# Optimization experiments

Measured on AMD Instinct MI355X. Metric: run time of the kernel, lower is better.

The kernel has to match this reference:

```python
import jax, jax.numpy as jnp
import numpy as np

B, N, T, D = 4, 256, 64, 128
DR, DH = 32, 128  # d_relation, d_hidden


def setup_inputs() -> dict:
    key = jax.random.key(0)
    ks = jax.random.split(key, 12)
    s = 0.05
    return {
        "H": jax.random.normal(ks[0], (B, N, T, D), jnp.float32),
        "R": jax.random.normal(ks[1], (B, N, N, DR), jnp.float32),
        "delta_H": jax.random.normal(ks[2], (B, N, T, D), jnp.float32),
        # params (torch Linear convention: W @ x + b with W shape (out, in))
        "Wq": jax.random.normal(ks[3], (DH, D), jnp.float32) * s,
        "bq": jnp.zeros((DH,), jnp.float32),
        "Wk": jax.random.normal(ks[4], (DH, D), jnp.float32) * s,
        "bk": jnp.zeros((DH,), jnp.float32),
        "Wr": jax.random.normal(ks[5], (DH, DR), jnp.float32) * s,
        "br": jnp.zeros((DH,), jnp.float32),
        "Wf": jax.random.normal(ks[6], (D, 3 * D + DR), jnp.float32) * s,
        "bf": jnp.zeros((D,), jnp.float32),
        "gamma": jnp.ones((D,), jnp.float32),
        "beta": jnp.zeros((D,), jnp.float32),
    }


def reference(H, R, delta_H, Wq, bq, Wk, bk, Wr, br, Wf, bf, gamma, beta):
    Bm, Nn, Tt, Dd = H.shape
    dr = R.shape[-1]

    # projections (eval mode: dropout is identity)
    q = jnp.einsum('bitd,hd->bith', H, Wq) + bq           # (B,N,T,DH)
    k = jnp.einsum('bjtd,hd->bjth', H, Wk) + bk           # (B,N,T,DH)
    rproj = jnp.einsum('bijr,hr->bijh', R, Wr) + br       # (B,N,N,DH)

    # attn_score[b,i,j,t] = <q_i[t], k_j[t] + Wr(r_ij)> / sqrt(d_model)
    scores = (jnp.einsum('bith,bjth->bijt', q, k)
              + jnp.einsum('bith,bijh->bijt', q, rproj)) / jnp.sqrt(jnp.asarray(Dd, H.dtype))
    w = jax.nn.softmax(scores, axis=-1)                   # softmax over time t
    # exclude the j == i pair (original loop skips it)
    w = w * (1.0 - jnp.eye(Nn, dtype=w.dtype))[None, :, :, None]

    # fuse Linear decomposed over the concat [h_i, h_j, r_ij, sum_t delta_h_j]
    W1 = Wf[:, :Dd]                 # acts on h_i
    W2 = Wf[:, Dd:2 * Dd]           # acts on h_j
    W3 = Wf[:, 2 * Dd:2 * Dd + dr]  # acts on r_ij
    W4 = Wf[:, 2 * Dd + dr:]        # acts on delta sum

    A = jnp.einsum('bitd,ed->bite', H, W1)                       # (B,N,T,D)
    Bj = jnp.einsum('bjtd,ed->bjte', H, W2)                      # (B,N,T,D)
    Cij = jnp.einsum('bijr,er->bije', R, W3)                     # (B,N,N,D)
    Ej = jnp.einsum('bjd,ed->bje', delta_H.sum(axis=2), W4)      # (B,N,D)

    wsum = w.sum(axis=2)                                         # (B,N,T)
    z = ((A + bf) * wsum[..., None]
         + jnp.einsum('bijt,bjte->bite', w, Bj)
         + jnp.einsum('bijt,bije->bite', w, Cij)
         + jnp.einsum('bijt,bje->bite', w, Ej))

    # residual + LayerNorm over last dim
    x = H + z
    mu = x.mean(axis=-1, keepdims=True)
    var = x.var(axis=-1, keepdims=True)
    return (x - mu) / jnp.sqrt(var + 1e-5) * gamma + beta
```

## Files before the change

kernel.cpp:

```cpp
#include <hip/hip_runtime.h>

typedef __attribute__((ext_vector_type(4))) float f32x4;
typedef __attribute__((ext_vector_type(8))) short short8;

constexpr int NB = 4, NS = 256, NT = 64, ND = 128, NR = 32;
constexpr int WFR = 3 * ND + NR;
constexpr float SCALE = 0.08838834764831845f;

__device__ __forceinline__ unsigned short f2bf(float f) {
  unsigned x = __float_as_uint(f);
  return (unsigned short)((x + 0x7FFFu + ((x >> 16) & 1u)) >> 16);
}
__device__ __forceinline__ float bf2f(unsigned short u) {
  return __uint_as_float((unsigned)u << 16);
}

__global__ __launch_bounds__(256) void kPrep(
    const float* __restrict__ Wq, const float* __restrict__ Wk,
    const float* __restrict__ Wr, const float* __restrict__ br,
    const float* __restrict__ bq, const float* __restrict__ Wf,
    const float* __restrict__ dH, const float* __restrict__ R,
    unsigned short* __restrict__ Wqb, unsigned short* __restrict__ Wkb,
    unsigned short* __restrict__ W1b, unsigned short* __restrict__ W2b,
    unsigned short* __restrict__ W3b, unsigned short* __restrict__ Wqrt,
    float* __restrict__ Gbias, float* __restrict__ Ej,
    unsigned short* __restrict__ Rb, unsigned short* __restrict__ Rtb) {
  __shared__ __align__(16) char smem[17408];
  const int blk = blockIdx.x, tid = threadIdx.x;
  if (blk < 116) {
    if (blk < 64) {
      const int which = blk >> 4;
      const int idx = ((blk & 15) * 256 + tid) * 4;
      const int e = idx >> 7, d = idx & 127;
      float4 v;
      unsigned short* dst;
      if (which == 0)      { v = *(const float4*)&Wq[idx];            dst = Wqb; }
      else if (which == 1) { v = *(const float4*)&Wk[idx];            dst = Wkb; }
      else if (which == 2) { v = *(const float4*)&Wf[e * WFR + d];        dst = W1b; }
      else                 { v = *(const float4*)&Wf[e * WFR + ND + d];   dst = W2b; }
      dst[idx + 0] = f2bf(v.x); dst[idx + 1] = f2bf(v.y);
      dst[idx + 2] = f2bf(v.z); dst[idx + 3] = f2bf(v.w);
    } else if (blk < 68) {
      const int idx = ((blk - 64) * 256 + tid) * 4;
      const int e = idx >> 5, r = idx & 31;
      float4 v = *(const float4*)&Wf[e * WFR + 2 * ND + r];
      W3b[idx + 0] = f2bf(v.x); W3b[idx + 1] = f2bf(v.y);
      W3b[idx + 2] = f2bf(v.z); W3b[idx + 3] = f2bf(v.w);
    } else {
      const int rr = blk - 68;
      float* Vl = (float*)smem;
      float* gbl = Vl + 128;
      if (tid < 128) {
        float v = 0.f;
        if (rr < 32) v = Wr[tid * 32 + rr];
        else if (rr == 32) v = br[tid];
        Vl[tid] = v;
        gbl[tid] = bq[tid] * v;
      }
      __syncthreads();
      if (tid < 128) {
        float acc = 0.f;
        #pragma unroll 8
        for (int h = 0; h < 128; ++h) acc += Wq[h * 128 + tid] * Vl[h];
        Wqrt[rr * 128 + tid] = f2bf(acc * SCALE);
      }
      if (tid == 0) {
        float g = 0.f;
        for (int h = 0; h < 128; ++h) g += gbl[h];
        Gbias[rr] = g * SCALE;
      }
    }
  } else if (blk < 628) {
    float* ds = (float*)smem;
    const int half = tid >> 7, d = tid & 127;
    const int bj = (blk - 116) * 2 + half;
    const float* p = dH + (size_t)bj * NT * ND + d;
    float s = 0.f;
    #pragma unroll 8
    for (int t = 0; t < NT; ++t) s += p[t * ND];
    ds[half * 128 + d] = s;
    __syncthreads();
    const float* w4 = Wf + (size_t)d * WFR + 2 * ND + NR;
    float acc = 0.f;
    #pragma unroll 8
    for (int dd = 0; dd < ND; ++dd) acc += ds[half * 128 + dd] * w4[dd];
    Ej[(size_t)bj * ND + d] = acc;
  } else {
    unsigned short* rt = (unsigned short*)smem;
    const int bi = blk - 628;
    const float* src = R + (size_t)bi * 8192;
    #pragma unroll
    for (int it = 0; it < 8; ++it) {
      const int idx = (tid + it * 256) * 4;
      const float4 v = *(const float4*)&src[idx];
      const unsigned short s0 = f2bf(v.x), s1 = f2bf(v.y);
      const unsigned short s2 = f2bf(v.z), s3 = f2bf(v.w);
      unsigned long long p = (unsigned long long)s0 | ((unsigned long long)s1 << 16)
                           | ((unsigned long long)s2 << 32) | ((unsigned long long)s3 << 48);
      *(unsigned long long*)&Rb[(size_t)bi * 8192 + idx] = p;
      const int j = idx >> 5, r = idx & 31;
      *(unsigned*)&rt[j * 34 + r]     = (unsigned)s0 | ((unsigned)s1 << 16);
      *(unsigned*)&rt[j * 34 + r + 2] = (unsigned)s2 | ((unsigned)s3 << 16);
    }
    __syncthreads();
    #pragma unroll
    for (int it = 0; it < 4; ++it) {
      const int flat = (tid + it * 256) * 8;
      const int r = flat >> 8, j0 = flat & 255;
      short8 o;
      #pragma unroll
      for (int u = 0; u < 8; ++u) o[u] = (short)rt[(j0 + u) * 34 + r];
      *(short8*)&Rtb[(size_t)bi * 8192 + flat] = o;
    }
  }
}

__device__ __forceinline__ void gemm_tile(const short8 (&afr)[4][4],
    const unsigned short* __restrict__ Wp, int nt, int l15, int l4,
    f32x4 (&acc)[4]) {
  #pragma unroll
  for (int mt = 0; mt < 4; ++mt) acc[mt] = (f32x4){0.f, 0.f, 0.f, 0.f};
  #pragma unroll
  for (int kt = 0; kt < 4; ++kt) {
    short8 bfr = *(const short8*)(Wp + (16 * nt + l15) * 128 + 32 * kt + 8 * l4);
    #pragma unroll
    for (int mt = 0; mt < 4; ++mt)
      acc[mt] = __builtin_amdgcn_mfma_f32_16x16x32_bf16(afr[mt][kt], bfr, acc[mt], 0, 0, 0);
  }
}

__device__ __forceinline__ void gemm_tile2(const short8 (&afr)[2][4],
    const unsigned short* __restrict__ Wp, int nt, int l15, int l4,
    f32x4 (&acc)[2]) {
  #pragma unroll
  for (int mt = 0; mt < 2; ++mt) acc[mt] = (f32x4){0.f, 0.f, 0.f, 0.f};
  #pragma unroll
  for (int kt = 0; kt < 4; ++kt) {
    short8 bfr = *(const short8*)(Wp + (16 * nt + l15) * 128 + 32 * kt + 8 * l4);
    #pragma unroll
    for (int mt = 0; mt < 2; ++mt)
      acc[mt] = __builtin_amdgcn_mfma_f32_16x16x32_bf16(afr[mt][kt], bfr, acc[mt], 0, 0, 0);
  }
}

__global__ __launch_bounds__(256) void kB(const float* __restrict__ H,
    const unsigned short* __restrict__ W1b, const unsigned short* __restrict__ W2b,
    const unsigned short* __restrict__ Wqrt, const float* __restrict__ Gbias,
    const float* __restrict__ bf, const float* __restrict__ Ej,
    unsigned short* __restrict__ Apbb, unsigned short* __restrict__ BEb,
    unsigned short* __restrict__ Gb, unsigned short* __restrict__ Ht) {
  __shared__ unsigned short st[2][64 * 136];
  const int bn = blockIdx.x, tid = threadIdx.x;
  const int b = bn >> 8, n = bn & 255;
  const int lane = tid & 63, wv = tid >> 6;
  const int l15 = lane & 15, l4 = lane >> 4;
  short8 afr[4][4];
  const float* hb = H + (size_t)bn * (NT * ND);
  #pragma unroll
  for (int mt = 0; mt < 4; ++mt)
    #pragma unroll
    for (int kt = 0; kt < 4; ++kt) {
      const float* p = hb + (16 * mt + l15) * ND + 32 * kt + 8 * l4;
      float4 u0 = *(const float4*)p;
      float4 u1 = *(const float4*)(p + 4);
      short8 f;
      f[0] = (short)f2bf(u0.x); f[1] = (short)f2bf(u0.y);
      f[2] = (short)f2bf(u0.z); f[3] = (short)f2bf(u0.w);
      f[4] = (short)f2bf(u1.x); f[5] = (short)f2bf(u1.y);
      f[6] = (short)f2bf(u1.z); f[7] = (short)f2bf(u1.w);
      afr[mt][kt] = f;
    }
  f32x4 acc[4];
  #pragma unroll 1
  for (int pass = 0; pass < 2; ++pass) {
    const unsigned short* W = (pass == 0) ? W1b : W2b;
    unsigned short* buf = st[pass];
    #pragma unroll
    for (int n2 = 0; n2 < 2; ++n2) {
      const int nt = 2 * wv + n2, c = 16 * nt + l15;
      gemm_tile(afr, W, nt, l15, l4, acc);
      const float bias = (pass == 0) ? bf[c] : Ej[(size_t)bn * 128 + c];
      #pragma unroll
      for (int mt = 0; mt < 4; ++mt)
        #pragma unroll
        for (int jr = 0; jr < 4; ++jr)
          buf[(16 * mt + 4 * l4 + jr) * 136 + c] = f2bf(acc[mt][jr] + bias);
    }
  }
  if (wv < 3) {
    const int nt = wv, c = 16 * nt + l15;
    gemm_tile(afr, Wqrt, nt, l15, l4, acc);
    const float bias = Gbias[c];
    #pragma unroll
    for (int mt = 0; mt < 4; ++mt)
      #pragma unroll
      for (int jr = 0; jr < 4; ++jr) {
        const int tr = 16 * mt + 4 * l4 + jr;
        Gb[(size_t)bn * 3072 + tr * 48 + c] = f2bf(acc[mt][jr] + bias);
      }
  }
  __syncthreads();
  #pragma unroll
  for (int it = 0; it < 4; ++it) {
    const int flat = tid * 8 + it * 2048;
    const int row = flat >> 7, col = flat & 127;
    *(short8*)&Apbb[(size_t)bn * 8192 + flat] = *(const short8*)&st[0][row * 136 + col];
    *(short8*)&BEb[((size_t)(b * 64 + row) * 256 + n) * 128 + col] =
        *(const short8*)&st[1][row * 136 + col];
  }
  __syncthreads();
  if (wv == 0) {
    #pragma unroll
    for (int mt = 0; mt < 4; ++mt)
      #pragma unroll
      for (int kt = 0; kt < 4; ++kt)
        *(short8*)&st[0][(16 * mt + l15) * 136 + 32 * kt + 8 * l4] = afr[mt][kt];
  }
  __syncthreads();
  #pragma unroll
  for (int it = 0; it < 4; ++it) {
    const int flat = tid * 8 + it * 2048;
    const int row = flat >> 7, col = flat & 127;
    *(short8*)&Ht[((size_t)(b * 64 + row) * 256 + n) * 128 + col] =
        *(const short8*)&st[0][row * 136 + col];
  }
}

__global__ __launch_bounds__(512) void kQK(const unsigned short* __restrict__ Ht,
    const unsigned short* __restrict__ Wqb, const unsigned short* __restrict__ Wkb,
    const float* __restrict__ bq, const float* __restrict__ bk,
    unsigned short* __restrict__ Sb) {
  __shared__ unsigned short qs[256 * 136];
  __shared__ unsigned short ks[256 * 136];
  const int bt = blockIdx.x;
  const int tid = threadIdx.x, lane = tid & 63, wv = tid >> 6;
  const int l15 = lane & 15, l4 = lane >> 4;
  const unsigned short* hsrc = Ht + (size_t)bt * (256 * 128);
  short8 afr[2][4];
  #pragma unroll
  for (int mt = 0; mt < 2; ++mt)
    #pragma unroll
    for (int kt = 0; kt < 4; ++kt) {
      const int n = 32 * wv + 16 * mt + l15;
      afr[mt][kt] = *(const short8*)(hsrc + n * 128 + 32 * kt + 8 * l4);
    }
  f32x4 acc[2];
  #pragma unroll 1
  for (int pass = 0; pass < 2; ++pass) {
    const unsigned short* W = (pass == 0) ? Wqb : Wkb;
    const float* bp = (pass == 0) ? bq : bk;
    unsigned short* dst = (pass == 0) ? qs : ks;
    #pragma unroll
    for (int nt = 0; nt < 8; ++nt) {
      gemm_tile2(afr, W, nt, l15, l4, acc);
      const int c = 16 * nt + l15;
      const float bias = bp[c];
      #pragma unroll
      for (int mt = 0; mt < 2; ++mt)
        #pragma unroll
        for (int jr = 0; jr < 4; ++jr)
          dst[(32 * wv + 16 * mt + 4 * l4 + jr) * 136 + c] = f2bf(acc[mt][jr] + bias);
    }
  }
  __syncthreads();
  short8 qa[2][4];
  #pragma unroll
  for (int mt = 0; mt < 2; ++mt)
    #pragma unroll
    for (int kt = 0; kt < 4; ++kt)
      qa[mt][kt] = *(const short8*)&qs[(32 * wv + 16 * mt + l15) * 136 + 32 * kt + 8 * l4];
  unsigned short* buf = qs + wv * (32 * 136);
  #pragma unroll 1
  for (int jh = 0; jh < 2; ++jh) {
    f32x4 sacc[2][8];
    #pragma unroll
    for (int mi = 0; mi < 2; ++mi)
      #pragma unroll
      for (int ntj = 0; ntj < 8; ++ntj) sacc[mi][ntj] = (f32x4){0.f, 0.f, 0.f, 0.f};
    #pragma unroll
    for (int kt = 0; kt < 4; ++kt) {
      short8 bb[8];
      #pragma unroll
      for (int ntj = 0; ntj < 8; ++ntj)
        bb[ntj] = *(const short8*)&ks[(16 * (8 * jh + ntj) + l15) * 136 + 32 * kt + 8 * l4];
      #pragma unroll
      for (int mi = 0; mi < 2; ++mi)
        #pragma unroll
        for (int ntj = 0; ntj < 8; ++ntj)
          sacc[mi][ntj] = __builtin_amdgcn_mfma_f32_16x16x32_bf16(qa[mi][kt], bb[ntj], sacc[mi][ntj], 0, 0, 0);
    }
    #pragma unroll
    for (int mi = 0; mi < 2; ++mi)
      #pragma unroll
      for (int ntj = 0; ntj < 8; ++ntj)
        #pragma unroll
        for (int jr = 0; jr < 4; ++jr)
          buf[(16 * mi + 4 * l4 + jr) * 136 + 16 * ntj + l15] =
              f2bf(sacc[mi][ntj][jr] * SCALE);
    #pragma unroll
    for (int it = 0; it < 8; ++it) {
      const int flat = lane * 8 + it * 512;
      const int row = flat >> 7, col = flat & 127;
      *(short8*)&Sb[((size_t)bt * 256 + 32 * wv + row) * 256 + 128 * jh + col] =
          *(const short8*)&buf[row * 136 + col];
    }
  }
}

__global__ __launch_bounds__(256) void kSM(
    const unsigned short* __restrict__ Gb, const unsigned short* __restrict__ Rb,
    const unsigned short* __restrict__ Rtb, const unsigned short* __restrict__ Sb,
    const unsigned short* __restrict__ W3b, const unsigned short* __restrict__ Apbb,
    unsigned short* __restrict__ Zt, unsigned short* __restrict__ Wbw) {
  __shared__ unsigned short wl[64 * 264];
  __shared__ unsigned short Ml[4][16 * 40];
  __shared__ float wred[4][64];
  __shared__ float wsl[64];
  const int bi = blockIdx.x, b = bi >> 8, i = bi & 255;
  const int tid = threadIdx.x, lane = tid & 63, wv = tid >> 6;
  const int l15 = lane & 15, l4 = lane >> 4;
  const f32x4 zz = (f32x4){0.f, 0.f, 0.f, 0.f};

  #pragma unroll
  for (int it = 0; it < 8; ++it) {
    const int flat = tid * 8 + it * 2048;
    const int t = flat >> 8, col = flat & 255;
    *(short8*)&wl[t * 264 + col] =
        *(const short8*)&Sb[(((size_t)b * 64 + t) * 256 + i) * 256 + col];
  }

  short8 ga[4];
  #pragma unroll
  for (int mt = 0; mt < 4; ++mt)
    ga[mt] = *(const short8*)(Gb + ((size_t)bi * 64 + 16 * mt + l15) * 48 + 8 * l4);
  f32x4 acc[4][4];
  #pragma unroll
  for (int nt = 0; nt < 4; ++nt) {
    const int j = 64 * wv + 16 * nt + l15;
    short8 rb = *(const short8*)(Rb + ((size_t)bi * 256 + j) * 32 + 8 * l4);
    #pragma unroll
    for (int mt = 0; mt < 4; ++mt)
      acc[mt][nt] = __builtin_amdgcn_mfma_f32_16x16x32_bf16(ga[mt], rb, zz, 0, 0, 0);
  }
  float qbr[4][4];
  #pragma unroll
  for (int mt = 0; mt < 4; ++mt)
    #pragma unroll
    for (int jr = 0; jr < 4; ++jr)
      qbr[mt][jr] = bf2f(Gb[((size_t)bi * 64 + 16 * mt + 4 * l4 + jr) * 48 + 32]);

  __syncthreads();

  #pragma unroll
  for (int mt = 0; mt < 4; ++mt)
    #pragma unroll
    for (int nt = 0; nt < 4; ++nt)
      #pragma unroll
      for (int jr = 0; jr < 4; ++jr)
        acc[mt][nt][jr] += bf2f(wl[(16 * mt + 4 * l4 + jr) * 264 + 64 * wv + 16 * nt + l15])
                         + qbr[mt][jr];

  #pragma unroll
  for (int nt = 0; nt < 4; ++nt) {
    float mx = -1e30f;
    #pragma unroll
    for (int mt = 0; mt < 4; ++mt)
      #pragma unroll
      for (int jr = 0; jr < 4; ++jr) mx = fmaxf(mx, acc[mt][nt][jr]);
    mx = fmaxf(mx, __shfl_xor(mx, 16));
    mx = fmaxf(mx, __shfl_xor(mx, 32));
    float sm = 0.f;
    #pragma unroll
    for (int mt = 0; mt < 4; ++mt)
      #pragma unroll
      for (int jr = 0; jr < 4; ++jr) {
        const float e = __expf(acc[mt][nt][jr] - mx);
        acc[mt][nt][jr] = e;
        sm += e;
      }
    sm += __shfl_xor(sm, 16);
    sm += __shfl_xor(sm, 32);
    const int j = 64 * wv + 16 * nt + l15;
    const float inv = (j == i) ? 0.f : 1.f / sm;
    #pragma unroll
    for (int mt = 0; mt < 4; ++mt)
      #pragma unroll
      for (int jr = 0; jr < 4; ++jr) acc[mt][nt][jr] *= inv;
  }

  float part[4][4];
  #pragma unroll
  for (int mt = 0; mt < 4; ++mt)
    #pragma unroll
    for (int jr = 0; jr < 4; ++jr) {
      float s = 0.f;
      #pragma unroll
      for (int nt = 0; nt < 4; ++nt) s += acc[mt][nt][jr];
      part[mt][jr] = s;
    }
  #pragma unroll
  for (int m = 1; m < 16; m <<= 1)
    #pragma unroll
    for (int mt = 0; mt < 4; ++mt)
      #pragma unroll
      for (int jr = 0; jr < 4; ++jr) part[mt][jr] += __shfl_xor(part[mt][jr], m);
  if (l15 == 0) {
    #pragma unroll
    for (int mt = 0; mt < 4; ++mt)
      #pragma unroll
      for (int jr = 0; jr < 4; ++jr) wred[wv][16 * mt + 4 * l4 + jr] = part[mt][jr];
  }

  #pragma unroll
  for (int mt = 0; mt < 4; ++mt)
    #pragma unroll
    for (int nt = 0; nt < 4; ++nt)
      #pragma unroll
      for (int jr = 0; jr < 4; ++jr)
        wl[(16 * mt + 4 * l4 + jr) * 264 + 64 * wv + 16 * nt + l15] =
            f2bf(acc[mt][nt][jr]);

  __syncthreads();

  if (tid < 64) wsl[tid] = wred[0][tid] + wred[1][tid] + wred[2][tid] + wred[3][tid];

  #pragma unroll
  for (int it = 0; it < 8; ++it) {
    const int flat = tid * 8 + it * 2048;
    const int t = flat >> 8, j = flat & 255;
    *(short8*)&Wbw[(((size_t)(b * 64 + t)) * 256 + i) * 256 + j] =
        *(const short8*)&wl[t * 264 + j];
  }

  f32x4 mac[2];
  mac[0] = zz; mac[1] = zz;
  #pragma unroll
  for (int kt = 0; kt < 8; ++kt) {
    short8 a = *(const short8*)&wl[(16 * wv + l15) * 264 + 32 * kt + 8 * l4];
    #pragma unroll
    for (int nt = 0; nt < 2; ++nt) {
      short8 bb = *(const short8*)(Rtb + ((size_t)bi * 32 + 16 * nt + l15) * 256 + 32 * kt + 8 * l4);
      mac[nt] = __builtin_amdgcn_mfma_f32_16x16x32_bf16(a, bb, mac[nt], 0, 0, 0);
    }
  }
  #pragma unroll
  for (int nt = 0; nt < 2; ++nt)
    #pragma unroll
    for (int jr = 0; jr < 4; ++jr)
      Ml[wv][(4 * l4 + jr) * 40 + 16 * nt + l15] = f2bf(mac[nt][jr]);
  asm volatile("s_waitcnt lgkmcnt(0)" ::: "memory");
  short8 a2 = *(const short8*)&Ml[wv][l15 * 40 + 8 * l4];
  f32x4 tac[8];
  #pragma unroll
  for (int nt = 0; nt < 8; ++nt) {
    short8 w3 = *(const short8*)(W3b + (16 * nt + l15) * 32 + 8 * l4);
    tac[nt] = __builtin_amdgcn_mfma_f32_16x16x32_bf16(a2, w3, zz, 0, 0, 0);
  }
  __syncthreads();

  const size_t abase = (size_t)bi * 8192;
  #pragma unroll
  for (int it = 0; it < 4; ++it) {
    const int flat = tid * 8 + it * 2048;
    const int row = flat >> 7, col = flat & 127;
    *(short8*)&wl[row * 136 + col] = *(const short8*)&Apbb[abase + flat];
  }
  __syncthreads();
  #pragma unroll
  for (int jr = 0; jr < 4; ++jr) {
    const int t = 16 * wv + 4 * l4 + jr;
    const float ws = wsl[t];
    #pragma unroll
    for (int nt = 0; nt < 8; ++nt) {
      const int e = 16 * nt + l15;
      const int off = t * 136 + e;
      wl[off] = f2bf(bf2f(wl[off]) * ws + tac[nt][jr]);
    }
  }
  __syncthreads();
  #pragma unroll
  for (int it = 0; it < 4; ++it) {
    const int flat = tid * 8 + it * 2048;
    const int row = flat >> 7, col = flat & 127;
    *(short8*)&Zt[((size_t)(b * 64 + row) * 256 + i) * 128 + col] =
        *(const short8*)&wl[row * 136 + col];
  }
}

__global__ __launch_bounds__(512) void kD(const unsigned short* __restrict__ Wb,
    const unsigned short* __restrict__ BEb, const unsigned short* __restrict__ Zt,
    const unsigned short* __restrict__ Ht, const float* __restrict__ gamma,
    const float* __restrict__ beta, float* __restrict__ out) {
  __shared__ unsigned short Bl[128 * 264];
  const int bt = blockIdx.x;
  const int b = bt >> 6, t = bt & 63;
  const int tid = threadIdx.x, lane = tid & 63, wv = tid >> 6;
  const int l15 = lane & 15, l4 = lane >> 4;
  {
    const int j = tid >> 1, eh = (tid & 1) * 64;
    const unsigned short* src = BEb + (size_t)bt * (256 * 128) + j * 128 + eh;
    #pragma unroll
    for (int eg = 0; eg < 8; ++eg) {
      short8 v = *(const short8*)(src + 8 * eg);
      #pragma unroll
      for (int u = 0; u < 8; ++u)
        Bl[(eh + 8 * eg + u) * 264 + j] = (unsigned short)v[u];
    }
  }
  __syncthreads();
  f32x4 acc[2][8];
  #pragma unroll
  for (int m2 = 0; m2 < 2; ++m2)
    #pragma unroll
    for (int nt = 0; nt < 8; ++nt) acc[m2][nt] = (f32x4){0.f, 0.f, 0.f, 0.f};
  #pragma unroll
  for (int kt = 0; kt < 8; ++kt) {
    short8 a[2];
    #pragma unroll
    for (int m2 = 0; m2 < 2; ++m2) {
      const int i = 32 * wv + 16 * m2 + l15;
      a[m2] = *(const short8*)(Wb + ((size_t)(b * 64 + t) * 256 + i) * 256 + 32 * kt + 8 * l4);
    }
    #pragma unroll
    for (int nt = 0; nt < 8; ++nt) {
      short8 bb = *(const short8*)(&Bl[(16 * nt + l15) * 264 + 32 * kt + 8 * l4]);
      #pragma unroll
      for (int m2 = 0; m2 < 2; ++m2)
        acc[m2][nt] = __builtin_amdgcn_mfma_f32_16x16x32_bf16(a[m2], bb, acc[m2][nt], 0, 0, 0);
    }
  }
  unsigned short* Zl = Bl;
  #pragma unroll 1
  for (int src = 0; src < 2; ++src) {
    const unsigned short* gsrc = (src == 0) ? Zt : Ht;
    __syncthreads();
    #pragma unroll
    for (int it = 0; it < 8; ++it) {
      const int flat = tid * 8 + it * 4096;
      const int row = flat >> 7, col = flat & 127;
      *(short8*)&Zl[row * 132 + col] =
          *(const short8*)&gsrc[((size_t)bt * 256 + row) * 128 + col];
    }
    __syncthreads();
    #pragma unroll
    for (int m2 = 0; m2 < 2; ++m2)
      #pragma unroll
      for (int jr = 0; jr < 4; ++jr) {
        const int i = 32 * wv + 16 * m2 + 4 * l4 + jr;
        #pragma unroll
        for (int nt = 0; nt < 8; ++nt)
          acc[m2][nt][jr] += bf2f(Zl[i * 132 + 16 * nt + l15]);
      }
  }
  float gam[8], bet[8];
  #pragma unroll
  for (int nt = 0; nt < 8; ++nt) {
    const int e = 16 * nt + l15;
    gam[nt] = gamma[e];
    bet[nt] = beta[e];
  }
  #pragma unroll
  for (int m2 = 0; m2 < 2; ++m2)
    #pragma unroll
    for (int jr = 0; jr < 4; ++jr) {
      const int i = 32 * wv + 16 * m2 + 4 * l4 + jr;
      const size_t base = ((size_t)(b * 256 + i) * 64 + t) * 128;
      float sm = 0.f, sq = 0.f;
      #pragma unroll
      for (int nt = 0; nt < 8; ++nt) {
        const float v = acc[m2][nt][jr];
        sm += v;
        sq += v * v;
      }
      #pragma unroll
      for (int m = 1; m < 16; m <<= 1) {
        sm += __shfl_xor(sm, m);
        sq += __shfl_xor(sq, m);
      }
      const float mu = sm * (1.f / 128.f);
      const float inv = rsqrtf(sq * (1.f / 128.f) - mu * mu + 1e-5f);
      #pragma unroll
      for (int nt = 0; nt < 8; ++nt)
        out[base + 16 * nt + l15] = (acc[m2][nt][jr] - mu) * inv * gam[nt] + bet[nt];
    }
}

extern "C" void kernel_launch(void* const* d_in, const int* in_sizes, int n_in,
                              void* d_out, int out_size, void* d_ws, size_t ws_size,
                              hipStream_t stream) {
  (void)in_sizes; (void)n_in; (void)out_size; (void)ws_size;
  const float* H     = (const float*)d_in[0];
  const float* R     = (const float*)d_in[1];
  const float* dH    = (const float*)d_in[2];
  const float* Wq    = (const float*)d_in[3];
  const float* bq    = (const float*)d_in[4];
  const float* Wk    = (const float*)d_in[5];
  const float* bk    = (const float*)d_in[6];
  const float* Wr    = (const float*)d_in[7];
  const float* br    = (const float*)d_in[8];
  const float* Wf    = (const float*)d_in[9];
  const float* bf    = (const float*)d_in[10];
  const float* gamma = (const float*)d_in[11];
  const float* beta  = (const float*)d_in[12];
  float* out = (float*)d_out;
  char* w = (char*)d_ws;

  unsigned short* Wbw  = (unsigned short*)(w + 0);
  unsigned short* Sb   = (unsigned short*)(w + 33554432);
  unsigned short* Apbb = (unsigned short*)(w + 67108864);
  unsigned short* BEb  = (unsigned short*)(w + 83886080);
  unsigned short* Gb   = (unsigned short*)(w + 100663296);
  unsigned short* Rb   = (unsigned short*)(w + 106954752);
  unsigned short* Rtb  = (unsigned short*)(w + 123731968);
  float*          Ejb  = (float*)(w + 140509184);
  unsigned short* Wqb  = (unsigned short*)(w + 141033472);
  unsigned short* Wkb  = (unsigned short*)(w + 141066240);
  unsigned short* W1b  = (unsigned short*)(w + 141099008);
  unsigned short* W2b  = (unsigned short*)(w + 141131776);
  unsigned short* W3b  = (unsigned short*)(w + 141164544);
  unsigned short* Wqrt = (unsigned short*)(w + 141172736);
  float*          Gbs  = (float*)(w + 141185024);
  unsigned short* Ht   = (unsigned short*)(w + 141185280);
  unsigned short* Zt   = (unsigned short*)(w + 157962496);

  kPrep<<<dim3(1652), dim3(256), 0, stream>>>(Wq, Wk, Wr, br, bq, Wf, dH, R,
                                              Wqb, Wkb, W1b, W2b, W3b, Wqrt,
                                              Gbs, Ejb, Rb, Rtb);
  kB<<<dim3(NB * NS), dim3(256), 0, stream>>>(H, W1b, W2b, Wqrt, Gbs,
                                              bf, Ejb, Apbb, BEb, Gb, Ht);
  kQK<<<dim3(NB * NT), dim3(512), 0, stream>>>(Ht, Wqb, Wkb, bq, bk, Sb);
  kSM<<<dim3(NB * NS), dim3(256), 0, stream>>>(Gb, Rb, Rtb, Sb, W3b, Apbb, Zt, Wbw);
  kD<<<dim3(NB * NT), dim3(512), 0, stream>>>(Wbw, BEb, Zt, Ht, gamma, beta, out);
}
```

Baseline: 142.9 us.

## Drop BE intermediate: recompute H·W2 in kD, add Ej term via MFMA in kSM

Removes the materialized BEb buffer (H·W2 + Ej, 16MB bf16 written by kB and read by kD). kD now computes H·W2 on the fly from the transposed Ht it already reads and writes the result into LDS. The Ej contribution is handled separately in kSM: Ej is stored transposed in bf16, and the w·Ej product is computed there with extra MFMAs. This saves a large global write/read round trip and one kB pass, at the cost of extra MFMA work and W2/Ejt loads in kD and kSM, plus some added bf16 rounding of Ej.

```diff
diff --git a/kernel.cpp b/kernel.cpp
--- a/kernel.cpp
+++ b/kernel.cpp
@@ -23,7 +23,7 @@
     unsigned short* __restrict__ Wqb, unsigned short* __restrict__ Wkb,
     unsigned short* __restrict__ W1b, unsigned short* __restrict__ W2b,
     unsigned short* __restrict__ W3b, unsigned short* __restrict__ Wqrt,
-    float* __restrict__ Gbias, float* __restrict__ Ej,
+    float* __restrict__ Gbias, unsigned short* __restrict__ Ejt,
     unsigned short* __restrict__ Rb, unsigned short* __restrict__ Rtb) {
   __shared__ __align__(16) char smem[17408];
   const int blk = blockIdx.x, tid = threadIdx.x;
@@ -74,6 +74,7 @@
     float* ds = (float*)smem;
     const int half = tid >> 7, d = tid & 127;
     const int bj = (blk - 116) * 2 + half;
+    const int b = bj >> 8, j = bj & 255;
     const float* p = dH + (size_t)bj * NT * ND + d;
     float s = 0.f;
     #pragma unroll 8
@@ -84,7 +85,7 @@
     float acc = 0.f;
     #pragma unroll 8
     for (int dd = 0; dd < ND; ++dd) acc += ds[half * 128 + dd] * w4[dd];
-    Ej[(size_t)bj * ND + d] = acc;
+    Ejt[((size_t)b * 128 + d) * 256 + j] = f2bf(acc);
   } else {
     unsigned short* rt = (unsigned short*)smem;
     const int bi = blk - 628;
@@ -144,11 +145,10 @@
 }
 
 __global__ __launch_bounds__(256) void kB(const float* __restrict__ H,
-    const unsigned short* __restrict__ W1b, const unsigned short* __restrict__ W2b,
-    const unsigned short* __restrict__ Wqrt, const float* __restrict__ Gbias,
-    const float* __restrict__ bf, const float* __restrict__ Ej,
-    unsigned short* __restrict__ Apbb, unsigned short* __restrict__ BEb,
-    unsigned short* __restrict__ Gb, unsigned short* __restrict__ Ht) {
+    const unsigned short* __restrict__ W1b, const unsigned short* __restrict__ Wqrt,
+    const float* __restrict__ Gbias, const float* __restrict__ bf,
+    unsigned short* __restrict__ Apbb, unsigned short* __restrict__ Gb,
+    unsigned short* __restrict__ Ht) {
   __shared__ unsigned short st[2][64 * 136];
   const int bn = blockIdx.x, tid = threadIdx.x;
   const int b = bn >> 8, n = bn & 255;
@@ -171,21 +171,16 @@
       afr[mt][kt] = f;
     }
   f32x4 acc[4];
-  #pragma unroll 1
-  for (int pass = 0; pass < 2; ++pass) {
-    const unsigned short* W = (pass == 0) ? W1b : W2b;
-    unsigned short* buf = st[pass];
-    #pragma unroll
-    for (int n2 = 0; n2 < 2; ++n2) {
-      const int nt = 2 * wv + n2, c = 16 * nt + l15;
-      gemm_tile(afr, W, nt, l15, l4, acc);
-      const float bias = (pass == 0) ? bf[c] : Ej[(size_t)bn * 128 + c];
-      #pragma unroll
-      for (int mt = 0; mt < 4; ++mt)
-        #pragma unroll
-        for (int jr = 0; jr < 4; ++jr)
-          buf[(16 * mt + 4 * l4 + jr) * 136 + c] = f2bf(acc[mt][jr] + bias);
-    }
+  #pragma unroll
+  for (int n2 = 0; n2 < 2; ++n2) {
+    const int nt = 2 * wv + n2, c = 16 * nt + l15;
+    gemm_tile(afr, W1b, nt, l15, l4, acc);
+    const float bias = bf[c];
+    #pragma unroll
+    for (int mt = 0; mt < 4; ++mt)
+      #pragma unroll
+      for (int jr = 0; jr < 4; ++jr)
+        st[0][(16 * mt + 4 * l4 + jr) * 136 + c] = f2bf(acc[mt][jr] + bias);
   }
   if (wv < 3) {
     const int nt = wv, c = 16 * nt + l15;
@@ -199,30 +194,21 @@
         Gb[(size_t)bn * 3072 + tr * 48 + c] = f2bf(acc[mt][jr] + bias);
       }
   }
+  if (wv == 0) {
+    #pragma unroll
+    for (int mt = 0; mt < 4; ++mt)
+      #pragma unroll
+      for (int kt = 0; kt < 4; ++kt)
+        *(short8*)&st[1][(16 * mt + l15) * 136 + 32 * kt + 8 * l4] = afr[mt][kt];
+  }
   __syncthreads();
   #pragma unroll
   for (int it = 0; it < 4; ++it) {
     const int flat = tid * 8 + it * 2048;
     const int row = flat >> 7, col = flat & 127;
     *(short8*)&Apbb[(size_t)bn * 8192 + flat] = *(const short8*)&st[0][row * 136 + col];
-    *(short8*)&BEb[((size_t)(b * 64 + row) * 256 + n) * 128 + col] =
+    *(short8*)&Ht[((size_t)(b * 64 + row) * 256 + n) * 128 + col] =
         *(const short8*)&st[1][row * 136 + col];
-  }
-  __syncthreads();
-  if (wv == 0) {
-    #pragma unroll
-    for (int mt = 0; mt < 4; ++mt)
-      #pragma unroll
-      for (int kt = 0; kt < 4; ++kt)
-        *(short8*)&st[0][(16 * mt + l15) * 136 + 32 * kt + 8 * l4] = afr[mt][kt];
-  }
-  __syncthreads();
-  #pragma unroll
-  for (int it = 0; it < 4; ++it) {
-    const int flat = tid * 8 + it * 2048;
-    const int row = flat >> 7, col = flat & 127;
-    *(short8*)&Ht[((size_t)(b * 64 + row) * 256 + n) * 128 + col] =
-        *(const short8*)&st[0][row * 136 + col];
   }
 }
 
@@ -310,8 +296,9 @@
 __global__ __launch_bounds__(256) void kSM(
     const unsigned short* __restrict__ Gb, const unsigned short* __restrict__ Rb,
     const unsigned short* __restrict__ Rtb, const unsigned short* __restrict__ Sb,
-    const unsigned short* __restrict__ W3b, const unsigned short* __restrict__ Apbb,
-    unsigned short* __restrict__ Zt, unsigned short* __restrict__ Wbw) {
+    const unsigned short* __restrict__ W3b, const unsigned short* __restrict__ Ejt,
+    const unsigned short* __restrict__ Apbb, unsigned short* __restrict__ Zt,
+    unsigned short* __restrict__ Wbw) {
   __shared__ unsigned short wl[64 * 264];
   __shared__ unsigned short Ml[4][16 * 40];
   __shared__ float wred[4][64];
@@ -434,6 +421,9 @@
 
   f32x4 mac[2];
   mac[0] = zz; mac[1] = zz;
+  f32x4 m2[8];
+  #pragma unroll
+  for (int nt = 0; nt < 8; ++nt) m2[nt] = zz;
   #pragma unroll
   for (int kt = 0; kt < 8; ++kt) {
     short8 a = *(const short8*)&wl[(16 * wv + l15) * 264 + 32 * kt + 8 * l4];
@@ -441,6 +431,11 @@
     for (int nt = 0; nt < 2; ++nt) {
       short8 bb = *(const short8*)(Rtb + ((size_t)bi * 32 + 16 * nt + l15) * 256 + 32 * kt + 8 * l4);
       mac[nt] = __builtin_amdgcn_mfma_f32_16x16x32_bf16(a, bb, mac[nt], 0, 0, 0);
+    }
+    #pragma unroll
+    for (int nt = 0; nt < 8; ++nt) {
+      short8 eb = *(const short8*)(Ejt + ((size_t)b * 128 + 16 * nt + l15) * 256 + 32 * kt + 8 * l4);
+      m2[nt] = __builtin_amdgcn_mfma_f32_16x16x32_bf16(a, eb, m2[nt], 0, 0, 0);
     }
   }
   #pragma unroll
@@ -474,7 +469,7 @@
     for (int nt = 0; nt < 8; ++nt) {
       const int e = 16 * nt + l15;
       const int off = t * 136 + e;
-      wl[off] = f2bf(bf2f(wl[off]) * ws + tac[nt][jr]);
+      wl[off] = f2bf(bf2f(wl[off]) * ws + tac[nt][jr] + m2[nt][jr]);
     }
   }
   __syncthreads();
@@ -488,24 +483,40 @@
 }
 
 __global__ __launch_bounds__(512) void kD(const unsigned short* __restrict__ Wb,
-    const unsigned short* __restrict__ BEb, const unsigned short* __restrict__ Zt,
-    const unsigned short* __restrict__ Ht, const float* __restrict__ gamma,
+    const unsigned short* __restrict__ Ht, const unsigned short* __restrict__ W2b,
+    const unsigned short* __restrict__ Zt, const float* __restrict__ gamma,
     const float* __restrict__ beta, float* __restrict__ out) {
   __shared__ unsigned short Bl[128 * 264];
   const int bt = blockIdx.x;
   const int b = bt >> 6, t = bt & 63;
   const int tid = threadIdx.x, lane = tid & 63, wv = tid >> 6;
   const int l15 = lane & 15, l4 = lane >> 4;
-  {
-    const int j = tid >> 1, eh = (tid & 1) * 64;
-    const unsigned short* src = BEb + (size_t)bt * (256 * 128) + j * 128 + eh;
-    #pragma unroll
-    for (int eg = 0; eg < 8; ++eg) {
-      short8 v = *(const short8*)(src + 8 * eg);
-      #pragma unroll
-      for (int u = 0; u < 8; ++u)
-        Bl[(eh + 8 * eg + u) * 264 + j] = (unsigned short)v[u];
-    }
+  const unsigned short* hsrc = Ht + (size_t)bt * (256 * 128);
+  short8 hfr[2][4];
+  #pragma unroll
+  for (int mt = 0; mt < 2; ++mt)
+    #pragma unroll
+    for (int kt = 0; kt < 4; ++kt) {
+      const int j = 32 * wv + 16 * mt + l15;
+      hfr[mt][kt] = *(const short8*)(hsrc + j * 128 + 32 * kt + 8 * l4);
+    }
+  #pragma unroll
+  for (int nt = 0; nt < 8; ++nt) {
+    f32x4 be[2];
+    be[0] = (f32x4){0.f, 0.f, 0.f, 0.f};
+    be[1] = (f32x4){0.f, 0.f, 0.f, 0.f};
+    #pragma unroll
+    for (int kt = 0; kt < 4; ++kt) {
+      short8 w2 = *(const short8*)(W2b + (16 * nt + l15) * 128 + 32 * kt + 8 * l4);
+      #pragma unroll
+      for (int mt = 0; mt < 2; ++mt)
+        be[mt] = __builtin_amdgcn_mfma_f32_16x16x32_bf16(hfr[mt][kt], w2, be[mt], 0, 0, 0);
+    }
+    #pragma unroll
+    for (int mt = 0; mt < 2; ++mt)
+      #pragma unroll
+      for (int jr = 0; jr < 4; ++jr)
+        Bl[(16 * nt + l15) * 264 + 32 * wv + 16 * mt + 4 * l4 + jr] = f2bf(be[mt][jr]);
   }
   __syncthreads();
   f32x4 acc[2][8];
@@ -608,27 +619,27 @@
   unsigned short* Wbw  = (unsigned short*)(w + 0);
   unsigned short* Sb   = (unsigned short*)(w + 33554432);
   unsigned short* Apbb = (unsigned short*)(w + 67108864);
-  unsigned short* BEb  = (unsigned short*)(w + 83886080);
-  unsigned short* Gb   = (unsigned short*)(w + 100663296);
-  unsigned short* Rb   = (unsigned short*)(w + 106954752);
-  unsigned short* Rtb  = (unsigned short*)(w + 123731968);
-  float*          Ejb  = (float*)(w + 140509184);
-  unsigned short* Wqb  = (unsigned short*)(w + 141033472);
-  unsigned short* Wkb  = (unsigned short*)(w + 141066240);
-  unsigned short* W1b  = (unsigned short*)(w + 141099008);
-  unsigned short* W2b  = (unsigned short*)(w + 141131776);
-  unsigned short* W3b  = (unsigned short*)(w + 141164544);
-  unsigned short* Wqrt = (unsigned short*)(w + 141172736);
-  float*          Gbs  = (float*)(w + 141185024);
-  unsigned short* Ht   = (unsigned short*)(w + 141185280);
-  unsigned short* Zt   = (unsigned short*)(w + 157962496);
+  unsigned short* Gb   = (unsigned short*)(w + 83886080);
+  unsigned short* Rb   = (unsigned short*)(w + 90177536);
+  unsigned short* Rtb  = (unsigned short*)(w + 106954752);
+  unsigned short* Ejt  = (unsigned short*)(w + 123731968);
+  unsigned short* Wqb  = (unsigned short*)(w + 123994112);
+  unsigned short* Wkb  = (unsigned short*)(w + 124026880);
+  unsigned short* W1b  = (unsigned short*)(w + 124059648);
+  unsigned short* W2b  = (unsigned short*)(w + 124092416);
+  unsigned short* W3b  = (unsigned short*)(w + 124125184);
+  unsigned short* Wqrt = (unsigned short*)(w + 124133376);
+  float*          Gbs  = (float*)(w + 124145664);
+  unsigned short* Ht   = (unsigned short*)(w + 124145856);
+  unsigned short* Zt   = (unsigned short*)(w + 140923072);
 
   kPrep<<<dim3(1652), dim3(256), 0, stream>>>(Wq, Wk, Wr, br, bq, Wf, dH, R,
                                               Wqb, Wkb, W1b, W2b, W3b, Wqrt,
-                                              Gbs, Ejb, Rb, Rtb);
-  kB<<<dim3(NB * NS), dim3(256), 0, stream>>>(H, W1b, W2b, Wqrt, Gbs,
-                                              bf, Ejb, Apbb, BEb, Gb, Ht);
+                                              Gbs, Ejt, Rb, Rtb);
+  kB<<<dim3(NB * NS), dim3(256), 0, stream>>>(H, W1b, Wqrt, Gbs, bf,
+                                              Apbb, Gb, Ht);
   kQK<<<dim3(NB * NT), dim3(512), 0, stream>>>(Ht, Wqb, Wkb, bq, bk, Sb);
-  kSM<<<dim3(NB * NS), dim3(256), 0, stream>>>(Gb, Rb, Rtb, Sb, W3b, Apbb, Zt, Wbw);
-  kD<<<dim3(NB * NT), dim3(512), 0, stream>>>(Wbw, BEb, Zt, Ht, gamma, beta, out);
-}
+  kSM<<<dim3(NB * NS), dim3(256), 0, stream>>>(Gb, Rb, Rtb, Sb, W3b, Ejt,
+                                               Apbb, Zt, Wbw);
+  kD<<<dim3(NB * NT), dim3(512), 0, stream>>>(Wbw, Ht, W2b, Zt, gamma, beta, out);
+}
```

Measured after the change: 167.9 us. 1.17x slower.
